# Performance work log

Hardware: AMD Instinct MI355X
Metric: run time of the kernel (lower is better)

The kernel has to match this reference:

```python
import jax, jax.numpy as jnp
import numpy as np

LOG2 = np.float32(np.log(2.0))

def _jsd_pos(p):
    # get_positive_expectation, measure='JSD', average=False
    return LOG2 - jax.nn.softplus(-p)

def setup_inputs() -> dict:
    key = jax.random.key(0)
    k1, k2, k3, k4, k5, k6 = jax.random.split(key, 6)
    N, G, D = 65536, 512, 256
    batch_1 = jnp.sort(jax.random.randint(k1, (N,), 0, G))
    batch_2 = jnp.sort(jax.random.randint(k2, (N,), 0, G))
    z1 = jax.random.normal(k3, (N, D), dtype=jnp.float32)
    z2 = jax.random.normal(k4, (N, D), dtype=jnp.float32)
    g1 = jax.random.normal(k5, (G, D), dtype=jnp.float32)
    g2 = jax.random.normal(k6, (G, D), dtype=jnp.float32)
    return {"batch_1": batch_1, "batch_2": batch_2, "z1": z1, "z2": z2, "g1": g1, "g2": g2}

def reference(batch_1, batch_2, z1, z2, g1, g2):
    # pos_mask scatter-build -> dense one-hot [N, G]
    pos_mask_1 = jax.nn.one_hot(batch_1, g1.shape[0], dtype=z1.dtype)
    pos_mask_2 = jax.nn.one_hot(batch_2, g2.shape[0], dtype=z2.dtype)
    # masked node-graph similarity matrices [N, G]
    self_sim_1 = (z1 @ g1.T) * pos_mask_1
    self_sim_2 = (z2 @ g2.T) * pos_mask_2
    cross_sim_12 = (z1 @ g2.T) * pos_mask_1
    cross_sim_21 = (z2 @ g1.T) * pos_mask_2
    # sep=True branch: per-node row sums, L2 distance over nodes
    self_js_11 = _jsd_pos(self_sim_1).sum(1)
    cross_js_12 = _jsd_pos(cross_sim_12).sum(1)
    self_js_22 = _jsd_pos(self_sim_2).sum(1)
    cross_js_21 = _jsd_pos(cross_sim_21).sum(1)
    L_1 = jnp.sqrt(jnp.sum((self_js_11 - cross_js_12) ** 2))
    L_2 = jnp.sqrt(jnp.sum((self_js_22 - cross_js_21) ** 2))
    return L_1 + L_2
```

## Files before the change

kernel.cpp:

```cpp
#include <hip/hip_runtime.h>
#include <math.h>

#define D 256
#define NBLOCKS 1024
#define WAVES 4
#define NPW 16

__device__ __forceinline__ float spn(float p) {
    return fmaxf(-p, 0.0f) + __logf(1.0f + __expf(-fabsf(p)));
}

__device__ __forceinline__ float dot4(float4 a, float4 b) {
    return a.x * b.x + a.y * b.y + a.z * b.z + a.w * b.w;
}

__device__ __forceinline__ float wave64_reduce(float x) {
    int t;
    t = __builtin_amdgcn_update_dpp(0, __builtin_bit_cast(int, x), 0x111, 0xf, 0xf, true);
    x += __builtin_bit_cast(float, t);
    t = __builtin_amdgcn_update_dpp(0, __builtin_bit_cast(int, x), 0x112, 0xf, 0xf, true);
    x += __builtin_bit_cast(float, t);
    t = __builtin_amdgcn_update_dpp(0, __builtin_bit_cast(int, x), 0x114, 0xf, 0xf, true);
    x += __builtin_bit_cast(float, t);
    t = __builtin_amdgcn_update_dpp(0, __builtin_bit_cast(int, x), 0x118, 0xf, 0xf, true);
    x += __builtin_bit_cast(float, t);
    t = __builtin_amdgcn_update_dpp(0, __builtin_bit_cast(int, x), 0x142, 0xa, 0xf, true);
    x += __builtin_bit_cast(float, t);
    t = __builtin_amdgcn_update_dpp(0, __builtin_bit_cast(int, x), 0x143, 0xc, 0xf, true);
    x += __builtin_bit_cast(float, t);
    return x;
}

__global__ __launch_bounds__(256) void jsd_dot_run_kernel(
    const int*   __restrict__ b1,
    const int*   __restrict__ b2,
    const float* __restrict__ z1,
    const float* __restrict__ z2,
    const float* __restrict__ g1,
    const float* __restrict__ g2,
    float*       __restrict__ partials)
{
    const int wave = threadIdx.x >> 6;
    const int lane = threadIdx.x & 63;
    const int w    = blockIdx.x * WAVES + wave;

    const int sbase = __builtin_amdgcn_readfirstlane(w * NPW);

    int i1v[NPW], i2v[NPW];
    #pragma unroll
    for (int j = 0; j < NPW; ++j) {
        i1v[j] = b1[sbase + j];
        i2v[j] = b2[sbase + j];
    }

    const float4* z1p = (const float4*)(z1 + (size_t)sbase * D);
    const float4* z2p = (const float4*)(z2 + (size_t)sbase * D);

    float acc1 = 0.0f, acc2 = 0.0f;

    int ci1 = -1, ci2 = -1;
    float4 w11, w12, w22, w21;

    float4 a1n = z1p[lane];
    float4 a2n = z2p[lane];

    #pragma unroll
    for (int j = 0; j < NPW; ++j) {
        const float4 a1 = a1n;
        const float4 a2 = a2n;
        if (j + 1 < NPW) {
            a1n = z1p[(j + 1) * (D / 4) + lane];
            a2n = z2p[(j + 1) * (D / 4) + lane];
        }

        const int i1 = i1v[j];
        const int i2 = i2v[j];
        if (i1 != ci1) {
            w11 = ((const float4*)(g1 + (size_t)i1 * D))[lane];
            w12 = ((const float4*)(g2 + (size_t)i1 * D))[lane];
            ci1 = i1;
        }
        if (i2 != ci2) {
            w22 = ((const float4*)(g2 + (size_t)i2 * D))[lane];
            w21 = ((const float4*)(g1 + (size_t)i2 * D))[lane];
            ci2 = i2;
        }

        float s11 = wave64_reduce(dot4(a1, w11));
        float c12 = wave64_reduce(dot4(a1, w12));
        float s22 = wave64_reduce(dot4(a2, w22));
        float c21 = wave64_reduce(dot4(a2, w21));

        if (lane == 63) {
            float d1 = spn(c12) - spn(s11);
            float d2 = spn(c21) - spn(s22);
            acc1 += d1 * d1;
            acc2 += d2 * d2;
        }
    }

    __shared__ float s1[WAVES], s2[WAVES];
    if (lane == 63) { s1[wave] = acc1; s2[wave] = acc2; }
    __syncthreads();

    if (threadIdx.x == 0) {
        float t1 = 0.0f, t2 = 0.0f;
        #pragma unroll
        for (int k = 0; k < WAVES; ++k) { t1 += s1[k]; t2 += s2[k]; }
        partials[blockIdx.x * 2 + 0] = t1;
        partials[blockIdx.x * 2 + 1] = t2;
    }
}

__global__ __launch_bounds__(256) void jsd_reduce_kernel(
    const float* __restrict__ partials,
    float*       __restrict__ out)
{
    const int tid  = threadIdx.x;
    const int wave = tid >> 6;
    const int lane = tid & 63;

    float a = 0.0f, b = 0.0f;
    #pragma unroll
    for (int i = 0; i < NBLOCKS / 256; ++i) {
        a += partials[(i * 256 + tid) * 2 + 0];
        b += partials[(i * 256 + tid) * 2 + 1];
    }

    a = wave64_reduce(a);
    b = wave64_reduce(b);

    __shared__ float s1[4], s2[4];
    if (lane == 63) { s1[wave] = a; s2[wave] = b; }
    __syncthreads();

    if (tid == 0) {
        float t1 = s1[0] + s1[1] + s1[2] + s1[3];
        float t2 = s2[0] + s2[1] + s2[2] + s2[3];
        out[0] = sqrtf(t1) + sqrtf(t2);
    }
}

extern "C" void kernel_launch(void* const* d_in, const int* in_sizes, int n_in,
                              void* d_out, int out_size, void* d_ws, size_t ws_size,
                              hipStream_t stream) {
    const int*   b1 = (const int*)  d_in[0];
    const int*   b2 = (const int*)  d_in[1];
    const float* z1 = (const float*)d_in[2];
    const float* z2 = (const float*)d_in[3];
    const float* g1 = (const float*)d_in[4];
    const float* g2 = (const float*)d_in[5];
    float* out      = (float*)d_out;
    float* partials = (float*)d_ws;

    jsd_dot_run_kernel<<<NBLOCKS, 256, 0, stream>>>(b1, b2, z1, z2, g1, g2, partials);
    jsd_reduce_kernel<<<1, 256, 0, stream>>>(partials, out);
}
```

Measured before the change: 159.3 us.

## Process two nodes per wave using half-wave reductions and doubled grid

Each wave now splits into two 32-lane halves, and each half handles one node row with 8 floats per lane. This replaces the 16-sequential-node loop with 4 iterations of 2 nodes, and the grid grows to 2048 blocks. Dot products use a 5-step half-wave DPP reduction and then a final 64-lane reduction of the accumulators. The change is meant to raise memory-level parallelism and shorten the serial reduction chain. In exchange, more blocks are launched and graph rows are reloaded whenever either half sees a new index.

Result: no change. 157.1 us (-1.4%).

```diff
diff --git a/kernel.cpp b/kernel.cpp
--- a/kernel.cpp
+++ b/kernel.cpp
@@ -2,9 +2,9 @@
 #include <math.h>
 
 #define D 256
-#define NBLOCKS 1024
-#define WAVES 4
-#define NPW 16
+#define BLOCKS 2048
+#define WPB 4
+#define GPW 4
 
 __device__ __forceinline__ float spn(float p) {
     return fmaxf(-p, 0.0f) + __logf(1.0f + __expf(-fabsf(p)));
@@ -14,24 +14,30 @@
     return a.x * b.x + a.y * b.y + a.z * b.z + a.w * b.w;
 }
 
-__device__ __forceinline__ float wave64_reduce(float x) {
-    int t;
-    t = __builtin_amdgcn_update_dpp(0, __builtin_bit_cast(int, x), 0x111, 0xf, 0xf, true);
-    x += __builtin_bit_cast(float, t);
-    t = __builtin_amdgcn_update_dpp(0, __builtin_bit_cast(int, x), 0x112, 0xf, 0xf, true);
-    x += __builtin_bit_cast(float, t);
-    t = __builtin_amdgcn_update_dpp(0, __builtin_bit_cast(int, x), 0x114, 0xf, 0xf, true);
-    x += __builtin_bit_cast(float, t);
-    t = __builtin_amdgcn_update_dpp(0, __builtin_bit_cast(int, x), 0x118, 0xf, 0xf, true);
-    x += __builtin_bit_cast(float, t);
-    t = __builtin_amdgcn_update_dpp(0, __builtin_bit_cast(int, x), 0x142, 0xa, 0xf, true);
-    x += __builtin_bit_cast(float, t);
-    t = __builtin_amdgcn_update_dpp(0, __builtin_bit_cast(int, x), 0x143, 0xc, 0xf, true);
-    x += __builtin_bit_cast(float, t);
+template<int CTRL, int ROWMASK>
+__device__ __forceinline__ float dpp_add(float x) {
+    int t = __builtin_amdgcn_update_dpp(0, __builtin_bit_cast(int, x), CTRL, ROWMASK, 0xf, true);
+    return x + __builtin_bit_cast(float, t);
+}
+
+__device__ __forceinline__ float red32(float x) {
+    x = dpp_add<0x111, 0xf>(x);
+    x = dpp_add<0x112, 0xf>(x);
+    x = dpp_add<0x114, 0xf>(x);
+    x = dpp_add<0x118, 0xf>(x);
+    x = dpp_add<0x142, 0xa>(x);
     return x;
 }
 
-__global__ __launch_bounds__(256) void jsd_dot_run_kernel(
+__device__ __forceinline__ float red64(float x) {
+    x = red32(x);
+    x = dpp_add<0x143, 0xc>(x);
+    return x;
+}
+
+struct ZR { float4 a1lo, a1hi, a2lo, a2hi; };
+
+__global__ __launch_bounds__(256) void jsd_dot_gqr_kernel(
     const int*   __restrict__ b1,
     const int*   __restrict__ b2,
     const float* __restrict__ z1,
@@ -42,56 +48,77 @@
 {
     const int wave = threadIdx.x >> 6;
     const int lane = threadIdx.x & 63;
-    const int w    = blockIdx.x * WAVES + wave;
+    const int sub  = lane >> 5;
+    const int fl   = lane & 31;
+    const bool tail = (fl == 31);
 
-    const int sbase = __builtin_amdgcn_readfirstlane(w * NPW);
+    const int w    = blockIdx.x * WPB + wave;
+    const int base = w * (GPW * 2);
 
-    int i1v[NPW], i2v[NPW];
-    #pragma unroll
-    for (int j = 0; j < NPW; ++j) {
-        i1v[j] = b1[sbase + j];
-        i2v[j] = b2[sbase + j];
-    }
+    const float* z1p = z1 + (size_t)(base + sub) * D + fl * 8;
+    const float* z2p = z2 + (size_t)(base + sub) * D + fl * 8;
 
-    const float4* z1p = (const float4*)(z1 + (size_t)sbase * D);
-    const float4* z2p = (const float4*)(z2 + (size_t)sbase * D);
+    ZR  zr[2];
+    int i1v[2], i2v[2];
+
+    zr[0].a1lo = ((const float4*)z1p)[0];
+    zr[0].a1hi = ((const float4*)z1p)[1];
+    zr[0].a2lo = ((const float4*)z2p)[0];
+    zr[0].a2hi = ((const float4*)z2p)[1];
+    i1v[0] = b1[base + sub];
+    i2v[0] = b2[base + sub];
+
+    float4 w11lo{}, w11hi{}, w12lo{}, w12hi{};
+    float4 w21lo{}, w21hi{}, w22lo{}, w22hi{};
+    int ci1 = -1, ci2 = -1;
 
     float acc1 = 0.0f, acc2 = 0.0f;
 
-    int ci1 = -1, ci2 = -1;
-    float4 w11, w12, w22, w21;
+    #pragma unroll
+    for (int g = 0; g < GPW; ++g) {
+        const int cur = g & 1;
+        const int nxt = cur ^ 1;
 
-    float4 a1n = z1p[lane];
-    float4 a2n = z2p[lane];
-
-    #pragma unroll
-    for (int j = 0; j < NPW; ++j) {
-        const float4 a1 = a1n;
-        const float4 a2 = a2n;
-        if (j + 1 < NPW) {
-            a1n = z1p[(j + 1) * (D / 4) + lane];
-            a2n = z2p[(j + 1) * (D / 4) + lane];
+        if (g + 1 < GPW) {
+            const float* p1 = z1p + (size_t)(g + 1) * 2 * D;
+            const float* p2 = z2p + (size_t)(g + 1) * 2 * D;
+            zr[nxt].a1lo = ((const float4*)p1)[0];
+            zr[nxt].a1hi = ((const float4*)p1)[1];
+            zr[nxt].a2lo = ((const float4*)p2)[0];
+            zr[nxt].a2hi = ((const float4*)p2)[1];
+            i1v[nxt] = b1[base + (g + 1) * 2 + sub];
+            i2v[nxt] = b2[base + (g + 1) * 2 + sub];
         }
 
-        const int i1 = i1v[j];
-        const int i2 = i2v[j];
-        if (i1 != ci1) {
-            w11 = ((const float4*)(g1 + (size_t)i1 * D))[lane];
-            w12 = ((const float4*)(g2 + (size_t)i1 * D))[lane];
+        const int i1 = i1v[cur];
+        const int i2 = i2v[cur];
+
+        if (__any(i1 != ci1)) {
+            const float* q = g1 + (size_t)i1 * D + fl * 8;
+            const float* r = g2 + (size_t)i1 * D + fl * 8;
+            w11lo = ((const float4*)q)[0]; w11hi = ((const float4*)q)[1];
+            w12lo = ((const float4*)r)[0]; w12hi = ((const float4*)r)[1];
             ci1 = i1;
         }
-        if (i2 != ci2) {
-            w22 = ((const float4*)(g2 + (size_t)i2 * D))[lane];
-            w21 = ((const float4*)(g1 + (size_t)i2 * D))[lane];
+        if (__any(i2 != ci2)) {
+            const float* q = g2 + (size_t)i2 * D + fl * 8;
+            const float* r = g1 + (size_t)i2 * D + fl * 8;
+            w22lo = ((const float4*)q)[0]; w22hi = ((const float4*)q)[1];
+            w21lo = ((const float4*)r)[0]; w21hi = ((const float4*)r)[1];
             ci2 = i2;
         }
 
-        float s11 = wave64_reduce(dot4(a1, w11));
-        float c12 = wave64_reduce(dot4(a1, w12));
-        float s22 = wave64_reduce(dot4(a2, w22));
-        float c21 = wave64_reduce(dot4(a2, w21));
+        float p11 = dot4(zr[cur].a1lo, w11lo) + dot4(zr[cur].a1hi, w11hi);
+        float p12 = dot4(zr[cur].a1lo, w12lo) + dot4(zr[cur].a1hi, w12hi);
+        float p22 = dot4(zr[cur].a2lo, w22lo) + dot4(zr[cur].a2hi, w22hi);
+        float p21 = dot4(zr[cur].a2lo, w21lo) + dot4(zr[cur].a2hi, w21hi);
 
-        if (lane == 63) {
+        float s11 = red32(p11);
+        float c12 = red32(p12);
+        float s22 = red32(p22);
+        float c21 = red32(p21);
+
+        if (tail) {
             float d1 = spn(c12) - spn(s11);
             float d2 = spn(c21) - spn(s22);
             acc1 += d1 * d1;
@@ -99,14 +126,17 @@
         }
     }
 
-    __shared__ float s1[WAVES], s2[WAVES];
+    acc1 = red64(acc1);
+    acc2 = red64(acc2);
+
+    __shared__ float s1[WPB], s2[WPB];
     if (lane == 63) { s1[wave] = acc1; s2[wave] = acc2; }
     __syncthreads();
 
     if (threadIdx.x == 0) {
         float t1 = 0.0f, t2 = 0.0f;
         #pragma unroll
-        for (int k = 0; k < WAVES; ++k) { t1 += s1[k]; t2 += s2[k]; }
+        for (int k = 0; k < WPB; ++k) { t1 += s1[k]; t2 += s2[k]; }
         partials[blockIdx.x * 2 + 0] = t1;
         partials[blockIdx.x * 2 + 1] = t2;
     }
@@ -122,13 +152,13 @@
 
     float a = 0.0f, b = 0.0f;
     #pragma unroll
-    for (int i = 0; i < NBLOCKS / 256; ++i) {
+    for (int i = 0; i < BLOCKS / 256; ++i) {
         a += partials[(i * 256 + tid) * 2 + 0];
         b += partials[(i * 256 + tid) * 2 + 1];
     }
 
-    a = wave64_reduce(a);
-    b = wave64_reduce(b);
+    a = red64(a);
+    b = red64(b);
 
     __shared__ float s1[4], s2[4];
     if (lane == 63) { s1[wave] = a; s2[wave] = b; }
@@ -153,6 +183,6 @@
     float* out      = (float*)d_out;
     float* partials = (float*)d_ws;
 
-    jsd_dot_run_kernel<<<NBLOCKS, 256, 0, stream>>>(b1, b2, z1, z2, g1, g2, partials);
+    jsd_dot_gqr_kernel<<<BLOCKS, 256, 0, stream>>>(b1, b2, z1, z2, g1, g2, partials);
     jsd_reduce_kernel<<<1, 256, 0, stream>>>(partials, out);
 }
```
